# Kernel optimization log

Hardware: AMD Instinct MI355X
Metric: run time of the kernel (lower is better)

The kernel has to match this reference:

```python
import jax, jax.numpy as jnp
import numpy as np

N, V, H, K = 65536, 200, 128, 32

def _corr_cols(a, B):
    # Pearson correlation between vector a [M] and each column of B [M, V]
    ac = a - a.mean()
    Bc = B - B.mean(axis=0)
    num = (ac[:, None] * Bc).sum(axis=0)
    den = jnp.sqrt((ac ** 2).sum() * (Bc ** 2).sum(axis=0))
    return jnp.nan_to_num(num / den, nan=0.0)

def _pairwise_features(tv, ti, cv, ci):
    # tv, ti: [N]; cv, ci: [N, V] -> features [V, 11]
    tvc = tv[:, None]
    both = (1.0 - ti)[:, None] * (1.0 - ci)
    n = both.sum(0) + 1e-8
    tmean = (tvc * both).sum(0) / n
    cmean = (cv * both).sum(0) / n
    tcent = (tvc - tmean) * both
    ccent = (cv - cmean) * both
    cov = (tcent * ccent).sum(0) / n
    tstd = jnp.sqrt((tcent ** 2).sum(0) / n + 1e-8)
    cstd = jnp.sqrt((ccent ** 2).sum(0) / n + 1e-8)
    corr = cov / (tstd * cstd + 1e-8)
    mi = -0.5 * jnp.log(1.0 - jnp.minimum(corr ** 2, 0.99) + 1e-8)
    tmin, tmax = tv.min(), tv.max()
    cmin, cmax = cv.min(0), cv.max(0)
    overlap = jnp.maximum(0.0, (jnp.minimum(tmax, cmax) - jnp.maximum(tmin, cmin)) / (jnp.maximum(tmax - tmin, cmax - cmin) + 1e-8))
    lag = _corr_cols(tv[1:], cv[:-1])       # corrcoef(candidate[:-1], target[1:])
    rev = _corr_cols(tv[:-1], cv[1:])       # corrcoef(target[:-1], candidate[1:])
    var_t = jnp.var(tv)
    coef = corr * jnp.std(tv) / (cv.std(0) + 1e-8)
    residual = tvc - coef * (cv - cv.mean(0))
    var_ratio = residual.var(0) / (var_t + 1e-8)
    intv = (ci > 0.5).astype(tv.dtype)
    t_int = (tvc * intv).sum(0) / (intv.sum(0) + 1e-8)
    t_no = (tvc * (1.0 - intv)).sum(0) / ((1.0 - intv).sum(0) + 1e-8)
    effect = jnp.abs(t_int - t_no)
    tr = jnp.argsort(jnp.argsort(tv)).astype(tv.dtype)
    cr = jnp.argsort(jnp.argsort(cv, axis=0), axis=0).astype(tv.dtype)
    rank_corr = _corr_cols(tr, cr)
    feats = jnp.stack([corr, jnp.abs(corr), corr ** 2, mi, overlap, effect,
                       rank_corr, jnp.sign(corr), lag, rev, var_ratio], axis=-1)
    return jnp.nan_to_num(feats, nan=0.0)

def _forward(target_embedding, node_embeddings, data, W_pair, b_pair, Wq, bq, Wk, bk,
             W1, b1, ln_scale, ln_offset, W2, b2, W3, b3, Wd, target_idx):
    n_vars = node_embeddings.shape[0]
    tv, ti = data[:, target_idx, 0], data[:, target_idx, 1]
    cv, ci = data[:, :, 0], data[:, :, 1]
    pf = _pairwise_features(tv, ti, cv, ci)                       # [V, 11]
    pf = jnp.where((jnp.arange(n_vars) == target_idx)[:, None], 0.0, pf)
    q = target_embedding @ Wq + bq                                # [K]
    k = node_embeddings @ Wk + bk + (pf @ W_pair + b_pair)        # [V, K]
    scores = (k @ q) / jnp.sqrt(jnp.asarray(float(K), dtype=q.dtype))
    te = jnp.broadcast_to(target_embedding, (n_vars, target_embedding.shape[0]))
    combined = jnp.concatenate([te, node_embeddings, pf * 10.0], axis=-1)  # [V, 2H+11]
    h = jax.nn.gelu(combined @ W1 + b1)
    mu = h.mean(-1, keepdims=True)
    var = ((h - mu) ** 2).mean(-1, keepdims=True)
    h = (h - mu) / jnp.sqrt(var + 1e-5) * ln_scale + ln_offset    # LayerNorm (haiku eps=1e-5)
    h = jax.nn.gelu(h @ W2 + b2)
    net = (h @ W3 + b3)[:, 0]
    direct = (pf[:, jnp.array([0, 8, 10])] @ Wd)[:, 0]
    return scores + net + 0.5 * direct

def setup_inputs():
    key = jax.random.key(0)
    ks = jax.random.split(key, 16)
    def vs_uniform(k, fan_in, shape):
        # hk.initializers.VarianceScaling(2.0, 'fan_in', 'uniform')
        lim = np.sqrt(6.0 / fan_in)
        return jax.random.uniform(k, shape, minval=-lim, maxval=lim, dtype=jnp.float32)
    vals = jax.random.normal(ks[0], (N, V), dtype=jnp.float32)
    intv = (jax.random.uniform(ks[1], (N, V)) < 0.1).astype(jnp.float32)
    data = jnp.stack([vals, intv, jnp.ones((N, V), jnp.float32)], axis=-1)  # [N, V, 3]
    return {
        'target_embedding': jax.random.normal(ks[2], (H,), dtype=jnp.float32),
        'node_embeddings': jax.random.normal(ks[3], (V, H), dtype=jnp.float32),
        'data': data,
        'W_pair': vs_uniform(ks[4], 11, (11, K)), 'b_pair': jnp.zeros((K,), jnp.float32),
        'Wq': vs_uniform(ks[5], H, (H, K)), 'bq': jnp.zeros((K,), jnp.float32),
        'Wk': vs_uniform(ks[6], H, (H, K)), 'bk': jnp.zeros((K,), jnp.float32),
        'W1': vs_uniform(ks[7], 2 * H + 11, (2 * H + 11, H)), 'b1': jnp.zeros((H,), jnp.float32),
        'ln_scale': jnp.ones((H,), jnp.float32), 'ln_offset': jnp.zeros((H,), jnp.float32),
        'W2': vs_uniform(ks[8], H, (H, H // 2)), 'b2': jnp.zeros((H // 2,), jnp.float32),
        'W3': vs_uniform(ks[9], H // 2, (H // 2, 1)), 'b3': jnp.zeros((1,), jnp.float32),
        'Wd': vs_uniform(ks[10], 3, (3, 1)),
        'target_idx': 0,
    }

def reference(target_embedding, node_embeddings, data, W_pair, b_pair, Wq, bq, Wk, bk,
              W1, b1, ln_scale, ln_offset, W2, b2, W3, b3, Wd, target_idx):
    return _forward(target_embedding, node_embeddings, data, W_pair, b_pair, Wq, bq, Wk, bk,
                    W1, b1, ln_scale, ln_offset, W2, b2, W3, b3, Wd, target_idx)
```

## Files before the change

kernel.cpp:

```cpp
#include <hip/hip_runtime.h>
#include <stdint.h>

#define N_ROWS 65536
#define NV 200
#define NH 128
#define NKD 32
#define NBKT 32768
#define NB2A 512
#define ROWS_ST 32

__device__ __forceinline__ uint32_t fkey(float x){
  uint32_t u = __float_as_uint(x);
  return (u & 0x80000000u) ? ~u : (u | 0x80000000u);
}

__global__ __launch_bounds__(256) void k_extract(
    const float* __restrict__ data, const int* __restrict__ tgt,
    float* __restrict__ tvArr, float* __restrict__ tiArr,
    unsigned int* __restrict__ histT, double* __restrict__ tvP){
  int i = blockIdx.x*256 + threadIdx.x;
  int tg = *tgt;
  float v  = data[(size_t)i*600 + tg*3 + 0];
  float ti = data[(size_t)i*600 + tg*3 + 1];
  tvArr[i] = v; tiArr[i] = ti;
  atomicAdd(&histT[fkey(v)>>17], 1u);
  double s = (double)v, ss = (double)v*(double)v;
  float mn = v, mx = v;
  for (int off=32; off; off>>=1){
    s  += __shfl_down(s,  off);
    ss += __shfl_down(ss, off);
    mn = fminf(mn, __shfl_down(mn, off));
    mx = fmaxf(mx, __shfl_down(mx, off));
  }
  __shared__ double sd[4][4];
  int w = threadIdx.x >> 6;
  if ((threadIdx.x & 63) == 0){ sd[w][0]=s; sd[w][1]=ss; sd[w][2]=mn; sd[w][3]=mx; }
  __syncthreads();
  if (threadIdx.x == 0){
    double S=0, SS=0, MN=sd[0][2], MX=sd[0][3];
    for (int q=0;q<4;q++){ S+=sd[q][0]; SS+=sd[q][1]; MN=fmin(MN,sd[q][2]); MX=fmax(MX,sd[q][3]); }
    double* p = tvP + (size_t)blockIdx.x*4;
    p[0]=S; p[1]=SS; p[2]=MN; p[3]=MX;
  }
}

__global__ __launch_bounds__(256) void k_comb_tv(const double* __restrict__ tvP,
                                                 double* __restrict__ tvStats){
  int t = threadIdx.x;
  double s = tvP[t*4+0], ss = tvP[t*4+1], mn = tvP[t*4+2], mx = tvP[t*4+3];
  for (int off=32; off; off>>=1){
    s  += __shfl_down(s,  off);
    ss += __shfl_down(ss, off);
    mn = fmin(mn, __shfl_down(mn, off));
    mx = fmax(mx, __shfl_down(mx, off));
  }
  __shared__ double sd[4][4];
  int w = t >> 6;
  if ((t & 63) == 0){ sd[w][0]=s; sd[w][1]=ss; sd[w][2]=mn; sd[w][3]=mx; }
  __syncthreads();
  if (t == 0){
    double S=0, SS=0, MN=sd[0][2], MX=sd[0][3];
    for (int q=0;q<4;q++){ S+=sd[q][0]; SS+=sd[q][1]; MN=fmin(MN,sd[q][2]); MX=fmax(MX,sd[q][3]); }
    tvStats[0]=S; tvStats[1]=SS; tvStats[2]=MN; tvStats[3]=MX;
  }
}

__global__ __launch_bounds__(256) void k_scan(unsigned int* __restrict__ histT){
  __shared__ unsigned int h[256*129];
  __shared__ unsigned int aux[256];
  int t = threadIdx.x;
  for (int idx=t; idx<NBKT; idx+=256) h[(idx>>7)*129 + (idx&127)] = histT[idx];
  __syncthreads();
  unsigned int s = 0;
  #pragma unroll 8
  for (int k=0;k<128;k++) s += h[t*129+k];
  aux[t] = s; __syncthreads();
  for (int off=1; off<256; off<<=1){
    unsigned int v = (t>=off) ? aux[t-off] : 0u;
    __syncthreads();
    aux[t] += v;
    __syncthreads();
  }
  unsigned int run = aux[t] - s;
  #pragma unroll 8
  for (int k=0;k<128;k++){
    unsigned int c = h[t*129+k];
    h[t*129+k] = __float_as_uint((float)run + 0.5f*((float)c - 1.f));
    run += c;
  }
  __syncthreads();
  for (int idx=t; idx<NBKT; idx+=256) histT[idx] = h[(idx>>7)*129 + (idx&127)];
}

__global__ __launch_bounds__(256) void k_trank(const float* __restrict__ tvArr,
                                               const unsigned int* __restrict__ histT,
                                               float* __restrict__ trArr){
  int i = blockIdx.x*256 + threadIdx.x;
  trArr[i] = __uint_as_float(histT[fkey(tvArr[i])>>17]);
}

__global__ __launch_bounds__(256, 4) void k_main(
    const float* __restrict__ data, const float* __restrict__ tvArr,
    const float* __restrict__ tiArr, uint16_t* __restrict__ bktT,
    float* __restrict__ colP){
  __shared__ float   cvS[ROWS_ST][201];
  __shared__ uint8_t ciS[ROWS_ST][204];
  __shared__ float   tvS[ROWS_ST+2];
  __shared__ float   tiS[ROWS_ST];
  int t = threadIdx.x, blk = blockIdx.x;
  double acc[13];
  #pragma unroll
  for (int s=0;s<13;s++) acc[s]=0.0;
  float cmin = 3.4e38f, cmax = -3.4e38f;

  for (int st=0; st<4; ++st){
    int i0 = blk*128 + st*ROWS_ST;
    const float4* rb = (const float4*)(data + (size_t)i0*600);
    #pragma unroll 2
    for (int k=0;k<19;k++){
      int f = t + k*256;
      if (f < 4800){
        float4 v = rb[f];
        int r  = f/150;
        int e4 = f - r*150;
        int m  = e4 % 3;
        int c0 = (4*e4)/3;
        if (m==0){ cvS[r][c0]=v.x; ciS[r][c0]=(uint8_t)(v.y>0.5f); cvS[r][c0+1]=v.w; }
        else if (m==1){ ciS[r][c0]=(uint8_t)(v.x>0.5f); cvS[r][c0+1]=v.z; ciS[r][c0+1]=(uint8_t)(v.w>0.5f); }
        else { cvS[r][c0+1]=v.y; ciS[r][c0+1]=(uint8_t)(v.z>0.5f); }
      }
    }
    if (t < ROWS_ST+2){ int i = i0 - 1 + t; tvS[t] = (i>=0 && i<N_ROWS) ? tvArr[i] : 0.f; }
    else if (t >= 64 && t < 64+ROWS_ST){ tiS[t-64] = tiArr[i0 + (t-64)]; }
    __syncthreads();
    if (t < NV){
      float facc[13];
      #pragma unroll
      for (int s=0;s<13;s++) facc[s]=0.f;
      for (int r=0;r<ROWS_ST;r++){
        float cv = cvS[r][t];
        float ci = (float)ciS[r][t];
        float tv = tvS[r+1], tvm = tvS[r], tvp = tvS[r+2];
        float ti = tiS[r];
        float b  = (1.f-ti)*(1.f-ci);
        facc[0]+=cv;        facc[1]+=cv*cv;     facc[2]+=tv*cv;
        facc[3]+=ci;        facc[4]+=tv*ci;
        facc[5]+=b;         facc[6]+=tv*b;      facc[7]+=cv*b;
        facc[8]+=tv*cv*b;   facc[9]+=tv*tv*b;   facc[10]+=cv*cv*b;
        facc[11]+=tvp*cv;   facc[12]+=tvm*cv;
        cmin = fminf(cmin, cv); cmax = fmaxf(cmax, cv);
      }
      #pragma unroll
      for (int s=0;s<13;s++) acc[s] += (double)facc[s];
    }
    {
      int r = t & 31, cb = t >> 5;
      for (int cc=cb; cc<NV; cc+=8){
        float cv = cvS[r][cc];
        bktT[(size_t)cc*N_ROWS + i0 + r] = (uint16_t)(fkey(cv)>>17);
      }
    }
    __syncthreads();
  }
  if (t < NV){
    float* dst = colP + ((size_t)t*NB2A + blk)*16;
    #pragma unroll
    for (int s=0;s<13;s++) dst[s] = (float)acc[s];
    dst[13]=cmin; dst[14]=cmax;
  }
}

__global__ __launch_bounds__(256) void k_comb_cols(const float* __restrict__ colP,
                                                   double* __restrict__ colStats){
  int j = blockIdx.x, t = threadIdx.x;
  double a[13];
  #pragma unroll
  for (int s=0;s<13;s++) a[s]=0.0;
  float mn = 3.4e38f, mx = -3.4e38f;
  for (int b=t; b<NB2A; b+=256){
    const float* p = colP + ((size_t)j*NB2A + b)*16;
    #pragma unroll
    for (int s=0;s<13;s++) a[s] += (double)p[s];
    mn = fminf(mn, p[13]); mx = fmaxf(mx, p[14]);
  }
  for (int off=32; off; off>>=1){
    #pragma unroll
    for (int s=0;s<13;s++) a[s] += __shfl_down(a[s], off);
    mn = fminf(mn, __shfl_down(mn, off));
    mx = fmaxf(mx, __shfl_down(mx, off));
  }
  __shared__ double sd[4][15];
  int w = t >> 6;
  if ((t & 63) == 0){
    #pragma unroll
    for (int s=0;s<13;s++) sd[w][s]=a[s];
    sd[w][13]=(double)mn; sd[w][14]=(double)mx;
  }
  __syncthreads();
  if (t == 0){
    double* d = colStats + (size_t)j*16;
    #pragma unroll
    for (int s=0;s<13;s++) d[s] = sd[0][s]+sd[1][s]+sd[2][s]+sd[3][s];
    double MN=sd[0][13], MX=sd[0][14];
    for (int q=1;q<4;q++){ MN=fmin(MN,sd[q][13]); MX=fmax(MX,sd[q][14]); }
    d[13]=MN; d[14]=MX;
  }
}

__global__ __launch_bounds__(512, 1) void k_rank(const uint16_t* __restrict__ bktT,
                                                 const float* __restrict__ trArr,
                                                 double* __restrict__ colStats){
  __shared__ unsigned int h[512*65];
  __shared__ unsigned int aux[512];
  __shared__ double daux[8];
  int t = threadIdx.x, j = blockIdx.x;
  const uint16_t* col = bktT + (size_t)j*N_ROWS;
  for (int idx=t; idx<512*65; idx+=512) h[idx]=0u;
  __syncthreads();
  for (int k=0;k<N_ROWS/512;k++){
    int b = (int)col[t + k*512];
    atomicAdd(&h[(b>>6)*65 + (b&63)], 1u);
  }
  __syncthreads();
  unsigned int s = 0;
  #pragma unroll 8
  for (int k=0;k<64;k++) s += h[t*65+k];
  aux[t]=s; __syncthreads();
  for (int off=1; off<512; off<<=1){
    unsigned int v = (t>=off) ? aux[t-off] : 0u;
    __syncthreads();
    aux[t] += v;
    __syncthreads();
  }
  unsigned int run = aux[t] - s;
  #pragma unroll 8
  for (int k=0;k<64;k++){
    unsigned int c = h[t*65+k];
    h[t*65+k] = __float_as_uint((float)run + 0.5f*((float)c - 1.f));
    run += c;
  }
  __syncthreads();
  double srr = 0.0;
  for (int k=0;k<N_ROWS/512;k++){
    int i = t + k*512;
    int b = (int)col[i];
    srr += (double)trArr[i] * (double)__uint_as_float(h[(b>>6)*65 + (b&63)]);
  }
  for (int off=32; off; off>>=1) srr += __shfl_down(srr, off);
  if ((t&63)==0) daux[t>>6] = srr;
  __syncthreads();
  if (t==0){
    double s8=0;
    for (int q=0;q<8;q++) s8 += daux[q];
    colStats[(size_t)j*16 + 15] = s8;
  }
}

__device__ __forceinline__ float gelu_t(float x){
  float x3 = x*x*x;
  return 0.5f*x*(1.f + tanhf(0.7978845608f*(x + 0.044715f*x3)));
}

__global__ __launch_bounds__(128) void k_head(
    const float* __restrict__ te, const float* __restrict__ ne, const float* __restrict__ data,
    const float* __restrict__ Wpair, const float* __restrict__ bpair,
    const float* __restrict__ Wq, const float* __restrict__ bq,
    const float* __restrict__ Wk, const float* __restrict__ bk,
    const float* __restrict__ W1, const float* __restrict__ b1,
    const float* __restrict__ lns, const float* __restrict__ lno,
    const float* __restrict__ W2, const float* __restrict__ b2,
    const float* __restrict__ W3, const float* __restrict__ b3,
    const float* __restrict__ Wd, const int* __restrict__ tgt,
    const double* __restrict__ colStats, const double* __restrict__ tvStats,
    const float* __restrict__ tvArr, float* __restrict__ out){
  int j = blockIdx.x, t = threadIdx.x;
  int tg = *tgt;
  const double* cs = colStats + (size_t)j*16;
  double S_c=cs[0], S_cc=cs[1], S_tc=cs[2], S_ci=cs[3], S_ti=cs[4], S_b=cs[5],
         S_tb=cs[6], S_cb=cs[7], S_tcb=cs[8], S_ttb=cs[9], S_ccb=cs[10], L=cs[11], R=cs[12];
  float cmin=(float)cs[13], cmax=(float)cs[14];
  double S_rr=cs[15];
  double S_t=tvStats[0], S_tt=tvStats[1];
  float tmin=(float)tvStats[2], tmax=(float)tvStats[3];
  float tv0=tvArr[0], tvN=tvArr[N_ROWS-1];
  float cv0=data[j*3], cvN=data[(size_t)(N_ROWS-1)*600 + j*3];
  const double Nd = (double)N_ROWS;
  double n = S_b + 1e-8;
  double tmean=S_tb/n, cmean=S_cb/n;
  double cov=(S_tcb - tmean*S_cb - cmean*S_tb + tmean*cmean*S_b)/n;
  double t2=S_ttb - 2.0*tmean*S_tb + tmean*tmean*S_b;
  double c2=S_ccb - 2.0*cmean*S_cb + cmean*cmean*S_b;
  double tstd=sqrt(t2/n + 1e-8), cstd=sqrt(c2/n + 1e-8);
  double corr = cov/(tstd*cstd + 1e-8);
  double mi = -0.5*log(1.0 - fmin(corr*corr, 0.99) + 1e-8);
  float ovn = fminf(tmax,cmax) - fmaxf(tmin,cmin);
  float ovd = fmaxf(tmax-tmin, cmax-cmin) + 1e-8f;
  float overlap = fmaxf(0.f, ovn/ovd);
  double M = Nd - 1.0;
  double Sa=S_t-(double)tv0, Saa=S_tt-(double)tv0*(double)tv0;
  double Sb2=S_c-(double)cvN, Sbb=S_cc-(double)cvN*(double)cvN;
  double lnum = L - Sa*Sb2/M;
  double lden2 = (Saa - Sa*Sa/M)*(Sbb - Sb2*Sb2/M);
  double lag = (lden2 > 0.0) ? lnum/sqrt(lden2) : 0.0;
  double Sa2=S_t-(double)tvN, Saa2=S_tt-(double)tvN*(double)tvN;
  double Sc2=S_c-(double)cv0, Scc2=S_cc-(double)cv0*(double)cv0;
  double rnum = R - Sa2*Sc2/M;
  double rden2 = (Saa2 - Sa2*Sa2/M)*(Scc2 - Sc2*Sc2/M);
  double rev = (rden2 > 0.0) ? rnum/sqrt(rden2) : 0.0;
  double var_t = S_tt/Nd - (S_t/Nd)*(S_t/Nd);
  double var_c = S_cc/Nd - (S_c/Nd)*(S_c/Nd);
  double coef = corr*sqrt(var_t)/(sqrt(var_c) + 1e-8);
  double covf = S_tc/Nd - (S_t/Nd)*(S_c/Nd);
  double var_res = var_t + coef*coef*var_c - 2.0*coef*covf;
  double var_ratio = var_res/(var_t + 1e-8);
  double t_int = S_ti/(S_ci + 1e-8);
  double t_no  = (S_t - S_ti)/((Nd - S_ci) + 1e-8);
  double effect = fabs(t_int - t_no);
  const double m_ = (Nd-1.0)*0.5;
  double rank_corr = (S_rr - Nd*m_*m_) / (Nd*(Nd*Nd-1.0)/12.0);
  float pf[11];
  pf[0]=(float)corr; pf[1]=(float)fabs(corr); pf[2]=(float)(corr*corr); pf[3]=(float)mi;
  pf[4]=overlap; pf[5]=(float)effect; pf[6]=(float)rank_corr;
  pf[7]=(float)((corr>0.0)-(corr<0.0)); pf[8]=(float)lag; pf[9]=(float)rev; pf[10]=(float)var_ratio;
  if (j == tg){
    #pragma unroll
    for (int q=0;q<11;q++) pf[q]=0.f;
  }
  const float* nej = ne + (size_t)j*NH;
  float h = b1[t];
  for (int e=0;e<NH;e++) h += te[e]*W1[e*NH + t];
  for (int e=0;e<NH;e++) h += nej[e]*W1[(NH+e)*NH + t];
  #pragma unroll
  for (int f=0;f<11;f++) h += 10.f*pf[f]*W1[(2*NH+f)*NH + t];
  h = gelu_t(h);
  __shared__ float redW[2];
  __shared__ float hnS[NH];
  __shared__ float h2S[64];
  float v = h;
  for (int off=32; off; off>>=1) v += __shfl_down(v, off);
  if ((t&63)==0) redW[t>>6]=v;
  __syncthreads();
  float mu = (redW[0]+redW[1])*(1.f/128.f);
  __syncthreads();
  float d = h - mu;
  v = d*d;
  for (int off=32; off; off>>=1) v += __shfl_down(v, off);
  if ((t&63)==0) redW[t>>6]=v;
  __syncthreads();
  float var = (redW[0]+redW[1])*(1.f/128.f);
  float hn = d/sqrtf(var + 1e-5f)*lns[t] + lno[t];
  hnS[t] = hn;
  __syncthreads();
  if (t < 64){
    float h2 = b2[t];
    for (int o=0;o<NH;o++) h2 += hnS[o]*W2[o*64 + t];
    h2S[t] = gelu_t(h2);
  }
  __syncthreads();
  float netv = 0.f, scv = 0.f;
  if (t < 64){
    float v2 = h2S[t]*W3[t];
    for (int off=32; off; off>>=1) v2 += __shfl_down(v2, off);
    if (t==0) netv = v2 + b3[0];
  }
  if (t < 32){
    float q = bq[t], k = bk[t] + bpair[t];
    for (int e=0;e<NH;e++){ q += te[e]*Wq[e*NKD + t]; k += nej[e]*Wk[e*NKD + t]; }
    #pragma unroll
    for (int f=0;f<11;f++) k += pf[f]*Wpair[f*NKD + t];
    float sc = k*q;
    for (int off=16; off; off>>=1) sc += __shfl_down(sc, off, 32);
    if (t==0) scv = sc/sqrtf(32.f);
  }
  if (t == 0){
    float direct = pf[0]*Wd[0] + pf[8]*Wd[1] + pf[10]*Wd[2];
    out[j] = scv + netv + 0.5f*direct;
  }
}

extern "C" void kernel_launch(void* const* d_in, const int* in_sizes, int n_in,
                              void* d_out, int out_size, void* d_ws, size_t ws_size,
                              hipStream_t stream) {
  const float* te    = (const float*)d_in[0];
  const float* ne    = (const float*)d_in[1];
  const float* data  = (const float*)d_in[2];
  const float* Wpair = (const float*)d_in[3];
  const float* bpair = (const float*)d_in[4];
  const float* Wq    = (const float*)d_in[5];
  const float* bq    = (const float*)d_in[6];
  const float* Wk    = (const float*)d_in[7];
  const float* bk    = (const float*)d_in[8];
  const float* W1    = (const float*)d_in[9];
  const float* b1    = (const float*)d_in[10];
  const float* lns   = (const float*)d_in[11];
  const float* lno   = (const float*)d_in[12];
  const float* W2    = (const float*)d_in[13];
  const float* b2    = (const float*)d_in[14];
  const float* W3    = (const float*)d_in[15];
  const float* b3    = (const float*)d_in[16];
  const float* Wd    = (const float*)d_in[17];
  const int*   tgt   = (const int*)d_in[18];
  float* out = (float*)d_out;

  char* ws = (char*)d_ws;
  size_t off = 0;
  auto alloc = [&](size_t bytes)->char*{
    char* p = ws + off;
    off = (off + bytes + 255) & ~(size_t)255;
    return p;
  };
  uint16_t*     bktT     = (uint16_t*)    alloc((size_t)NV*N_ROWS*2);
  float*        tvArr    = (float*)       alloc(N_ROWS*4);
  float*        tiArr    = (float*)       alloc(N_ROWS*4);
  float*        trArr    = (float*)       alloc(N_ROWS*4);
  unsigned int* histT    = (unsigned int*)alloc(NBKT*4);
  double*       tvP      = (double*)      alloc(256*4*8);
  double*       tvStats  = (double*)      alloc(4*8);
  float*        colP     = (float*)       alloc((size_t)NV*NB2A*16*4);
  double*       colStats = (double*)      alloc((size_t)NV*16*8);
  if (off > ws_size) return;

  hipMemsetAsync(histT, 0, NBKT*4, stream);
  k_extract<<<dim3(N_ROWS/256), dim3(256), 0, stream>>>(data, tgt, tvArr, tiArr, histT, tvP);
  k_comb_tv<<<dim3(1), dim3(256), 0, stream>>>(tvP, tvStats);
  k_scan<<<dim3(1), dim3(256), 0, stream>>>(histT);
  k_trank<<<dim3(N_ROWS/256), dim3(256), 0, stream>>>(tvArr, histT, trArr);
  k_main<<<dim3(NB2A), dim3(256), 0, stream>>>(data, tvArr, tiArr, bktT, colP);
  k_comb_cols<<<dim3(NV), dim3(256), 0, stream>>>(colP, colStats);
  k_rank<<<dim3(NV), dim3(512), 0, stream>>>(bktT, trArr, colStats);
  k_head<<<dim3(NV), dim3(128), 0, stream>>>(te, ne, data, Wpair, bpair, Wq, bq, Wk, bk,
                                             W1, b1, lns, lno, W2, b2, W3, b3, Wd, tgt,
                                             colStats, tvStats, tvArr, out);
}
```

Before: 419.3 us.

## Split k_main into one 32-row tile per block with batched prefetch loads

Each k_main block now handles a single 32-row tile instead of looping over four, so the grid has four times as many blocks. All float4 loads for the tile are issued into registers before the shared-memory scatter, which raises memory-level parallelism. The per-block double accumulators are dropped. This quadruples the per-column partials written to colP that k_comb_cols must reduce, and the 19-float4 register array may raise register pressure.

```diff
diff --git a/kernel.cpp b/kernel.cpp
--- a/kernel.cpp
+++ b/kernel.cpp
@@ -6,8 +6,8 @@
 #define NH 128
 #define NKD 32
 #define NBKT 32768
-#define NB2A 512
-#define ROWS_ST 32
+#define ROWS_B 32
+#define NB2A (N_ROWS/ROWS_B)
 
 __device__ __forceinline__ uint32_t fkey(float x){
   uint32_t u = __float_as_uint(x);
@@ -103,70 +103,67 @@
     const float* __restrict__ data, const float* __restrict__ tvArr,
     const float* __restrict__ tiArr, uint16_t* __restrict__ bktT,
     float* __restrict__ colP){
-  __shared__ float   cvS[ROWS_ST][201];
-  __shared__ uint8_t ciS[ROWS_ST][204];
-  __shared__ float   tvS[ROWS_ST+2];
-  __shared__ float   tiS[ROWS_ST];
+  __shared__ float   cvS[ROWS_B][201];
+  __shared__ uint8_t ciS[ROWS_B][204];
+  __shared__ float   tvS[ROWS_B+2];
+  __shared__ float   tiS[ROWS_B];
   int t = threadIdx.x, blk = blockIdx.x;
-  double acc[13];
+  int i0 = blk*ROWS_B;
+
+  const float4* rb = (const float4*)(data + (size_t)i0*600);
+  float4 vals[19];
   #pragma unroll
-  for (int s=0;s<13;s++) acc[s]=0.0;
-  float cmin = 3.4e38f, cmax = -3.4e38f;
-
-  for (int st=0; st<4; ++st){
-    int i0 = blk*128 + st*ROWS_ST;
-    const float4* rb = (const float4*)(data + (size_t)i0*600);
-    #pragma unroll 2
-    for (int k=0;k<19;k++){
-      int f = t + k*256;
-      if (f < 4800){
-        float4 v = rb[f];
-        int r  = f/150;
-        int e4 = f - r*150;
-        int m  = e4 % 3;
-        int c0 = (4*e4)/3;
-        if (m==0){ cvS[r][c0]=v.x; ciS[r][c0]=(uint8_t)(v.y>0.5f); cvS[r][c0+1]=v.w; }
-        else if (m==1){ ciS[r][c0]=(uint8_t)(v.x>0.5f); cvS[r][c0+1]=v.z; ciS[r][c0+1]=(uint8_t)(v.w>0.5f); }
-        else { cvS[r][c0+1]=v.y; ciS[r][c0+1]=(uint8_t)(v.z>0.5f); }
-      }
+  for (int k=0;k<18;k++) vals[k] = rb[t + k*256];
+  if (t < 192) vals[18] = rb[t + 18*256];
+  if (t < ROWS_B+2){ int i = i0 - 1 + t; tvS[t] = (i>=0 && i<N_ROWS) ? tvArr[i] : 0.f; }
+  else if (t >= 64 && t < 64+ROWS_B){ tiS[t-64] = tiArr[i0 + (t-64)]; }
+
+  #pragma unroll
+  for (int k=0;k<19;k++){
+    int f = t + k*256;
+    if (k < 18 || t < 192){
+      float4 v = vals[k];
+      int r  = f/150;
+      int e4 = f - r*150;
+      int m  = e4 % 3;
+      int c0 = (4*e4)/3;
+      if (m==0){ cvS[r][c0]=v.x; ciS[r][c0]=(uint8_t)(v.y>0.5f); cvS[r][c0+1]=v.w; }
+      else if (m==1){ ciS[r][c0]=(uint8_t)(v.x>0.5f); cvS[r][c0+1]=v.z; ciS[r][c0+1]=(uint8_t)(v.w>0.5f); }
+      else { cvS[r][c0+1]=v.y; ciS[r][c0+1]=(uint8_t)(v.z>0.5f); }
     }
-    if (t < ROWS_ST+2){ int i = i0 - 1 + t; tvS[t] = (i>=0 && i<N_ROWS) ? tvArr[i] : 0.f; }
-    else if (t >= 64 && t < 64+ROWS_ST){ tiS[t-64] = tiArr[i0 + (t-64)]; }
-    __syncthreads();
-    if (t < NV){
-      float facc[13];
-      #pragma unroll
-      for (int s=0;s<13;s++) facc[s]=0.f;
-      for (int r=0;r<ROWS_ST;r++){
-        float cv = cvS[r][t];
-        float ci = (float)ciS[r][t];
-        float tv = tvS[r+1], tvm = tvS[r], tvp = tvS[r+2];
-        float ti = tiS[r];
-        float b  = (1.f-ti)*(1.f-ci);
-        facc[0]+=cv;        facc[1]+=cv*cv;     facc[2]+=tv*cv;
-        facc[3]+=ci;        facc[4]+=tv*ci;
-        facc[5]+=b;         facc[6]+=tv*b;      facc[7]+=cv*b;
-        facc[8]+=tv*cv*b;   facc[9]+=tv*tv*b;   facc[10]+=cv*cv*b;
-        facc[11]+=tvp*cv;   facc[12]+=tvm*cv;
-        cmin = fminf(cmin, cv); cmax = fmaxf(cmax, cv);
-      }
-      #pragma unroll
-      for (int s=0;s<13;s++) acc[s] += (double)facc[s];
+  }
+  __syncthreads();
+
+  if (t < NV){
+    float facc[13];
+    #pragma unroll
+    for (int s=0;s<13;s++) facc[s]=0.f;
+    float cmin = 3.4e38f, cmax = -3.4e38f;
+    for (int r=0;r<ROWS_B;r++){
+      float cv = cvS[r][t];
+      float ci = (float)ciS[r][t];
+      float tv = tvS[r+1], tvm = tvS[r], tvp = tvS[r+2];
+      float ti = tiS[r];
+      float b  = (1.f-ti)*(1.f-ci);
+      facc[0]+=cv;        facc[1]+=cv*cv;     facc[2]+=tv*cv;
+      facc[3]+=ci;        facc[4]+=tv*ci;
+      facc[5]+=b;         facc[6]+=tv*b;      facc[7]+=cv*b;
+      facc[8]+=tv*cv*b;   facc[9]+=tv*tv*b;   facc[10]+=cv*cv*b;
+      facc[11]+=tvp*cv;   facc[12]+=tvm*cv;
+      cmin = fminf(cmin, cv); cmax = fmaxf(cmax, cv);
     }
-    {
-      int r = t & 31, cb = t >> 5;
-      for (int cc=cb; cc<NV; cc+=8){
-        float cv = cvS[r][cc];
-        bktT[(size_t)cc*N_ROWS + i0 + r] = (uint16_t)(fkey(cv)>>17);
-      }
+    float* dst = colP + ((size_t)t*NB2A + blk)*16;
+    #pragma unroll
+    for (int s=0;s<13;s++) dst[s] = facc[s];
+    dst[13]=cmin; dst[14]=cmax;
+  }
+
+  {
+    int r = t & 31, cb = t >> 5;
+    for (int cc=cb; cc<NV; cc+=8){
+      float cv = cvS[r][cc];
+      bktT[(size_t)cc*N_ROWS + i0 + r] = (uint16_t)(fkey(cv)>>17);
     }
-    __syncthreads();
-  }
-  if (t < NV){
-    float* dst = colP + ((size_t)t*NB2A + blk)*16;
-    #pragma unroll
-    for (int s=0;s<13;s++) dst[s] = (float)acc[s];
-    dst[13]=cmin; dst[14]=cmax;
   }
 }
 
```

After: 410.6 us. -2.1%, faster.
